# Optimization experiments

Hardware: AMD Instinct MI355X
Metric: run time of the kernel (lower is better)

## Reference

```python
import jax, jax.numpy as jnp
import numpy as np

B, S, DMODEL, HEADS = 2, 2048, 1024, 16
DK = DMODEL // HEADS
DV = DMODEL // HEADS


def setup_inputs() -> dict:
    key = jax.random.key(0)
    kx, kq, kk, kv = jax.random.split(key, 4)
    x = jax.random.normal(kx, (B, S, DMODEL), dtype=jnp.float32)
    # stacked per-head projection weights, shape [H, dmodel, dk/dv]
    # (equivalent to nn.Linear(dmodel, dk, bias=False) per head)
    scale = 1.0 / np.sqrt(DMODEL)
    Wq = jax.random.uniform(kq, (HEADS, DMODEL, DK), jnp.float32, -scale, scale)
    Wk = jax.random.uniform(kk, (HEADS, DMODEL, DK), jnp.float32, -scale, scale)
    Wv = jax.random.uniform(kv, (HEADS, DMODEL, DV), jnp.float32, -scale, scale)
    return {"x": x, "Wq": Wq, "Wk": Wk, "Wv": Wv}


def reference(x, Wq, Wk, Wv):
    # per-head projections, batched across heads: [B,H,S,dk]
    q = jnp.einsum("bsd,hdk->bhsk", x, Wq)
    k = jnp.einsum("bsd,hdk->bhsk", x, Wk)
    v = jnp.einsum("bsd,hdv->bhsv", x, Wv)
    # NOTE: original module applies NO 1/sqrt(dk) scaling — keep faithful
    scores = jnp.einsum("bhqk,bhsk->bhqs", q, k)  # [B,H,S,S]
    attn = jax.nn.softmax(scores, axis=-1)
    out = jnp.einsum("bhqs,bhsv->bhqv", attn, v)  # [B,H,S,dv]
    # concat heads along last dim in head order
    Bsz, H, Sq, Dv = out.shape
    return jnp.transpose(out, (0, 2, 1, 3)).reshape(Bsz, Sq, H * Dv)
```

## Files before the change

### kernel.cpp

```cpp
#include <hip/hip_runtime.h>

#define B_ 2
#define S_ 2048
#define D_ 1024
#define H_ 16
#define DK_ 64
#define M_ (B_ * S_)
#define N_ (3 * D_)

typedef __bf16 bf16x8 __attribute__((ext_vector_type(8)));
typedef short s8vec __attribute__((ext_vector_type(8)));
typedef float f4vec __attribute__((ext_vector_type(4)));

static __device__ __forceinline__ ushort f2b(float f) {
  union { float f; unsigned u; } v; v.f = f;
  unsigned u = v.u;
  u += 0x7FFFu + ((u >> 16) & 1u);
  return (ushort)(u >> 16);
}

static __device__ __forceinline__ unsigned pk2(float a, float b) {
#if __has_builtin(__builtin_amdgcn_cvt_pk_bf16_f32)
  typedef __bf16 b2 __attribute__((ext_vector_type(2)));
  b2 r = __builtin_amdgcn_cvt_pk_bf16_f32(a, b);
  return __builtin_bit_cast(unsigned, r);
#else
  return (unsigned)f2b(a) | ((unsigned)f2b(b) << 16);
#endif
}

static __device__ __forceinline__ float fexp2(float x) {
#if __has_builtin(__builtin_amdgcn_exp2f)
  return __builtin_amdgcn_exp2f(x);
#else
  return exp2f(x);
#endif
}

static __device__ __forceinline__ f4vec mfma16(s8vec a, s8vec b, f4vec c) {
  return __builtin_amdgcn_mfma_f32_16x16x32_bf16(
      __builtin_bit_cast(bf16x8, a), __builtin_bit_cast(bf16x8, b), c, 0, 0, 0);
}

static __device__ __forceinline__ void gl_lds16(const ushort* g, ushort* l) {
  __builtin_amdgcn_global_load_lds(
      (const __attribute__((address_space(1))) unsigned*)g,
      (__attribute__((address_space(3))) unsigned*)l, 16, 0, 0);
}

static __device__ __forceinline__ void wg_barrier_lds() {
  asm volatile("" ::: "memory");
  __builtin_amdgcn_s_waitcnt(0xC07F);
  __builtin_amdgcn_s_barrier();
  asm volatile("" ::: "memory");
}

__global__ __launch_bounds__(256) void cvt_all(const float* __restrict__ x,
                                               const float* __restrict__ Wq,
                                               const float* __restrict__ Wk,
                                               const float* __restrict__ Wv,
                                               ushort* __restrict__ xb,
                                               ushort* __restrict__ wbt) {
  const int t = threadIdx.x;
  if (blockIdx.x < 4096) {
    int i = blockIdx.x * 256 + t;
    float4 v = ((const float4*)x)[i];
    ushort4 o;
    o.x = f2b(v.x); o.y = f2b(v.y); o.z = f2b(v.z); o.w = f2b(v.w);
    ((ushort4*)xb)[i] = o;
  } else {
    __shared__ ushort T[64 * 72];
    int bid = blockIdx.x - 4096;
    int w = bid >> 8, rem = bid & 255;
    int h = rem >> 4, d0 = (rem & 15) * 64;
    const float* W = (w == 0) ? Wq : (w == 1) ? Wk : Wv;
    const float* src = W + (size_t)h * 65536 + (size_t)d0 * 64;
#pragma unroll
    for (int j = 0; j < 4; ++j) {
      int idx = j * 256 + t;
      int dr = idx >> 4, kc = (idx & 15) * 4;
      float4 v = *(const float4*)(src + dr * 64 + kc);
      T[(kc + 0) * 72 + dr] = f2b(v.x);
      T[(kc + 1) * 72 + dr] = f2b(v.y);
      T[(kc + 2) * 72 + dr] = f2b(v.z);
      T[(kc + 3) * 72 + dr] = f2b(v.w);
    }
    __syncthreads();
    const int kk = t >> 2, dcg = (t & 3) * 16;
    ushort* dst = wbt + ((size_t)w * 1024 + h * 64 + kk) * 1024 + d0 + dcg;
    *(s8vec*)dst       = *(const s8vec*)&T[kk * 72 + dcg];
    *(s8vec*)(dst + 8) = *(const s8vec*)&T[kk * 72 + dcg + 8];
  }
}

__global__ __launch_bounds__(256) void proj_gemm(const ushort* __restrict__ xb,
                                                 const ushort* __restrict__ wbt,
                                                 ushort* __restrict__ qkv) {
  __shared__ __attribute__((aligned(16))) ushort As[128 * 64];
  __shared__ __attribute__((aligned(16))) ushort Bs[128 * 64];
  const int tid = threadIdx.x, wid = tid >> 6, lane = tid & 63;
  const int quad = lane >> 4, l15 = lane & 15;
  const int wm = wid & 1, wn = wid >> 1;
  const int m0 = blockIdx.x * 128, n0 = blockIdx.y * 128;

  f4vec acc[4][4];
#pragma unroll
  for (int mb = 0; mb < 4; mb++)
#pragma unroll
    for (int nb = 0; nb < 4; nb++)
#pragma unroll
      for (int i = 0; i < 4; i++) acc[mb][nb][i] = 0.f;

  const int sr = tid >> 3, sg = tid & 7;
  const int lg = sg ^ (sr & 7);
  const ushort* Ab = xb + (size_t)m0 * D_;
  const ushort* Bb = wbt + (size_t)n0 * D_;

  for (int k0 = 0; k0 < D_; k0 += 64) {
    __syncthreads();
#pragma unroll
    for (int j = 0; j < 4; ++j) {
      int r = j * 32 + sr;
      gl_lds16(Ab + (size_t)r * D_ + k0 + lg * 8, &As[j * 2048 + wid * 512]);
      gl_lds16(Bb + (size_t)r * D_ + k0 + lg * 8, &Bs[j * 2048 + wid * 512]);
    }
    __syncthreads();

#pragma unroll
    for (int kb = 0; kb < 2; ++kb) {
      s8vec af[4], bf[4];
#pragma unroll
      for (int mb = 0; mb < 4; ++mb) {
        int m = wm * 64 + mb * 16 + l15;
        int gpos = (kb * 4 + quad) ^ (m & 7);
        af[mb] = *(const s8vec*)&As[m * 64 + gpos * 8];
      }
#pragma unroll
      for (int nb = 0; nb < 4; ++nb) {
        int n = wn * 64 + nb * 16 + l15;
        int gpos = (kb * 4 + quad) ^ (n & 7);
        bf[nb] = *(const s8vec*)&Bs[n * 64 + gpos * 8];
      }
#pragma unroll
      for (int mb = 0; mb < 4; ++mb)
#pragma unroll
        for (int nb = 0; nb < 4; ++nb)
          acc[mb][nb] = mfma16(af[mb], bf[nb], acc[mb][nb]);
    }
  }

  const size_t per = (size_t)B_ * H_ * S_ * DK_;
  const int w = n0 >> 10;
  if (w == 2) {
    ushort* vt = qkv + 2 * per;
#pragma unroll
    for (int mb = 0; mb < 4; ++mb)
#pragma unroll
      for (int nb = 0; nb < 4; ++nb)
#pragma unroll
        for (int i = 0; i < 4; ++i) {
          int m = m0 + wm * 64 + mb * 16 + quad * 4 + i;
          int b = m >> 11, s = m & 2047;
          int n1 = (n0 & 1023) + wn * 64 + nb * 16 + l15;
          vt[((size_t)b * 1024 + n1) * S_ + s] = f2b(acc[mb][nb][i]);
        }
  } else {
    const float qs = (w == 0) ? 1.44269504f : 1.0f;
#pragma unroll
    for (int mb = 0; mb < 4; ++mb)
#pragma unroll
      for (int nb = 0; nb < 4; ++nb)
#pragma unroll
        for (int i = 0; i < 4; ++i) {
          int m = m0 + wm * 64 + mb * 16 + quad * 4 + i;
          int b = m >> 11, s = m & 2047;
          int n1 = (n0 & 1023) + wn * 64 + nb * 16 + l15;
          qkv[(size_t)w * per + (((size_t)b * H_ + (n1 >> 6)) * S_ + s) * 64 + (n1 & 63)] =
              f2b(acc[mb][nb][i] * qs);
        }
  }
}

__global__ __launch_bounds__(256) void attn(const ushort* __restrict__ qg,
                                            const ushort* __restrict__ kg,
                                            const ushort* __restrict__ vtg,
                                            float* __restrict__ out) {
  __shared__ __attribute__((aligned(16))) ushort Ks[64 * 64];
  __shared__ __attribute__((aligned(16))) ushort Vt[64 * 64];
  __shared__ __attribute__((aligned(16))) ushort Ps[4][32 * 128];
  const int qt = blockIdx.x, bh = blockIdx.y;
  const int b = bh >> 4, h = bh & 15;
  const int tid = threadIdx.x, wid = tid >> 6, lane = tid & 63;
  const int quad = lane >> 4, l15 = lane & 15, l7 = l15 & 7;

  const ushort* qbase = qg + ((size_t)bh * S_ + qt * 128 + wid * 32) * DK_;
  s8vec aq[2][2];
#pragma unroll
  for (int mb = 0; mb < 2; mb++) {
    aq[mb][0] = *(const s8vec*)(qbase + (size_t)(mb * 16 + l15) * DK_ + quad * 8);
    aq[mb][1] = *(const s8vec*)(qbase + (size_t)(mb * 16 + l15) * DK_ + 32 + quad * 8);
  }

  f4vec o[2][4];
  float lsum[2];
#pragma unroll
  for (int mb = 0; mb < 2; mb++) {
    lsum[mb] = 0.f;
#pragma unroll
    for (int nb = 0; nb < 4; nb++)
#pragma unroll
      for (int i = 0; i < 4; i++) o[mb][nb][i] = 0.f;
  }

  const int r = tid >> 3, gs = tid & 7;
  const int gk = gs ^ (r & 7);
  const ushort* kb_ = kg + (size_t)bh * S_ * DK_;
  const ushort* vb_ = vtg + (size_t)bh * 64 * S_;

  s8vec kpre[2], vpre[2];
  kpre[0] = *(const s8vec*)(kb_ + (size_t)r * DK_ + gk * 8);
  kpre[1] = *(const s8vec*)(kb_ + (size_t)(r + 32) * DK_ + gk * 8);
  vpre[0] = *(const s8vec*)(vb_ + (size_t)r * S_ + gk * 8);
  vpre[1] = *(const s8vec*)(vb_ + (size_t)(r + 32) * S_ + gk * 8);

  for (int kt = 0; kt < S_ / 64; ++kt) {
    wg_barrier_lds();
    *(s8vec*)&Ks[r * 64 + gs * 8]        = kpre[0];
    *(s8vec*)&Ks[(r + 32) * 64 + gs * 8] = kpre[1];
    *(s8vec*)&Vt[r * 64 + gs * 8]        = vpre[0];
    *(s8vec*)&Vt[(r + 32) * 64 + gs * 8] = vpre[1];
    if (kt + 1 < S_ / 64) {
      const ushort* kn = kb_ + (size_t)((kt + 1) * 64 + r) * DK_ + gk * 8;
      kpre[0] = *(const s8vec*)(kn);
      kpre[1] = *(const s8vec*)(kn + (size_t)32 * DK_);
      const ushort* vn = vb_ + (size_t)r * S_ + (kt + 1) * 64 + gk * 8;
      vpre[0] = *(const s8vec*)(vn);
      vpre[1] = *(const s8vec*)(vn + (size_t)32 * S_);
    }
    wg_barrier_lds();

    f4vec sct[2][4];
#pragma unroll
    for (int nb = 0; nb < 4; nb++) {
      const int row = nb * 16 + l15;
      s8vec ak0 = *(const s8vec*)&Ks[row * 64 + ((0 + quad) ^ l7) * 8];
      s8vec ak1 = *(const s8vec*)&Ks[row * 64 + ((4 + quad) ^ l7) * 8];
#pragma unroll
      for (int mb = 0; mb < 2; mb++) {
        f4vec z;
#pragma unroll
        for (int i = 0; i < 4; i++) z[i] = 0.f;
        z = mfma16(ak0, aq[mb][0], z);
        sct[mb][nb] = mfma16(ak1, aq[mb][1], z);
      }
    }

#pragma unroll
    for (int mb = 0; mb < 2; mb++) {
      const int q = mb * 16 + l15;
#pragma unroll
      for (int nb = 0; nb < 4; nb++) {
#pragma unroll
        for (int i = 0; i < 4; i++) {
          float p = fexp2(sct[mb][nb][i]);
          sct[mb][nb][i] = p;
          lsum[mb] += p;
        }
        unsigned p01 = pk2(sct[mb][nb][0], sct[mb][nb][1]);
        unsigned p23 = pk2(sct[mb][nb][2], sct[mb][nb][3]);
        const int c = (nb * 2 + (quad >> 1)) ^ l7;
        *(uint2*)&Ps[wid][q * 128 + c * 8 + (quad & 1) * 4] = make_uint2(p01, p23);
      }
    }

#pragma unroll
    for (int kc = 0; kc < 2; kc++) {
      s8vec ap[2];
#pragma unroll
      for (int mb = 0; mb < 2; mb++)
        ap[mb] = *(const s8vec*)&Ps[wid][(mb * 16 + l15) * 128 + (((kc * 4 + quad)) ^ l7) * 8];
#pragma unroll
      for (int nb = 0; nb < 4; nb++) {
        s8vec av = *(const s8vec*)&Vt[(nb * 16 + l15) * 64 + ((kc * 4 + quad) ^ l7) * 8];
        o[0][nb] = mfma16(av, ap[0], o[0][nb]);
        o[1][nb] = mfma16(av, ap[1], o[1][nb]);
      }
    }
  }

#pragma unroll
  for (int mb = 0; mb < 2; mb++) {
    lsum[mb] += __shfl_xor(lsum[mb], 16, 64);
    lsum[mb] += __shfl_xor(lsum[mb], 32, 64);
  }

#pragma unroll
  for (int mb = 0; mb < 2; mb++) {
    const float inv = 1.0f / lsum[mb];
    float* ob = out + ((size_t)b * S_ + qt * 128 + wid * 32 + mb * 16 + l15) * D_ + h * DK_;
#pragma unroll
    for (int nb = 0; nb < 4; nb++) {
      float4 v;
      v.x = o[mb][nb][0] * inv;
      v.y = o[mb][nb][1] * inv;
      v.z = o[mb][nb][2] * inv;
      v.w = o[mb][nb][3] * inv;
      *(float4*)(ob + nb * 16 + quad * 4) = v;
    }
  }
}

extern "C" void kernel_launch(void* const* d_in, const int* in_sizes, int n_in,
                              void* d_out, int out_size, void* d_ws, size_t ws_size,
                              hipStream_t stream) {
  const float* x  = (const float*)d_in[0];
  const float* Wq = (const float*)d_in[1];
  const float* Wk = (const float*)d_in[2];
  const float* Wv = (const float*)d_in[3];
  float* out = (float*)d_out;

  ushort* xb  = (ushort*)d_ws;
  ushort* wbt = xb + (size_t)B_ * S_ * D_;
  ushort* qkv = wbt + (size_t)3 * D_ * D_;
  const size_t per = (size_t)B_ * H_ * S_ * DK_;

  cvt_all<<<4096 + 768, 256, 0, stream>>>(x, Wq, Wk, Wv, xb, wbt);
  proj_gemm<<<dim3(M_ / 128, N_ / 128), 256, 0, stream>>>(xb, wbt, qkv);
  attn<<<dim3(S_ / 128, B_ * H_), 256, 0, stream>>>(qkv, qkv + per, qkv + 2 * per, out);
}
```

Baseline: 177.5 us.

## Stage projection epilogue through LDS and shrink attention blocks with MFMA row sums

The projection GEMM epilogue now writes results into shared memory and then emits 16-byte coalesced stores for Q, K and the transposed V, replacing scattered 2-byte global stores. The attention kernel drops to 128 threads and 64 query rows per block, doubling the grid and cutting LDS use. It also computes the softmax denominator by appending a block of ones to V so an extra MFMA column yields the row sum, which removes the per-element scalar adds and the final shuffle reductions. The costs are one extra MFMA per V tile, smaller per-block reuse of each loaded K/V tile, and a changed workspace layout.

```diff
diff --git a/kernel.cpp b/kernel.cpp
--- a/kernel.cpp
+++ b/kernel.cpp
@@ -96,8 +96,9 @@
 __global__ __launch_bounds__(256) void proj_gemm(const ushort* __restrict__ xb,
                                                  const ushort* __restrict__ wbt,
                                                  ushort* __restrict__ qkv) {
-  __shared__ __attribute__((aligned(16))) ushort As[128 * 64];
-  __shared__ __attribute__((aligned(16))) ushort Bs[128 * 64];
+  __shared__ __attribute__((aligned(16))) ushort BUF[2 * 128 * 64];
+  ushort* As = BUF;
+  ushort* Bs = BUF + 128 * 64;
   const int tid = threadIdx.x, wid = tid >> 6, lane = tid & 63;
   const int quad = lane >> 4, l15 = lane & 15;
   const int wm = wid & 1, wn = wid >> 1;
@@ -149,51 +150,80 @@
     }
   }
 
+  __syncthreads();
+  ushort* T = BUF + wid * 4096;
   const size_t per = (size_t)B_ * H_ * S_ * DK_;
   const int w = n0 >> 10;
+  const int sb = m0 + wm * 64;
+  const int b = sb >> 11;
+  const int nb0 = (n0 & 1023) + wn * 64;
+
   if (w == 2) {
+#pragma unroll
+    for (int mb = 0; mb < 4; ++mb) {
+      const int mc = mb * 2 + (quad >> 1);
+      const int moff = (quad & 1) * 4;
+#pragma unroll
+      for (int nb = 0; nb < 4; ++nb) {
+        const int np = nb * 16 + l15;
+        unsigned p01 = pk2(acc[mb][nb][0], acc[mb][nb][1]);
+        unsigned p23 = pk2(acc[mb][nb][2], acc[mb][nb][3]);
+        *(uint2*)&T[np * 64 + ((mc ^ (np & 7)) * 8) + moff] = make_uint2(p01, p23);
+      }
+    }
     ushort* vt = qkv + 2 * per;
 #pragma unroll
-    for (int mb = 0; mb < 4; ++mb)
-#pragma unroll
-      for (int nb = 0; nb < 4; ++nb)
-#pragma unroll
-        for (int i = 0; i < 4; ++i) {
-          int m = m0 + wm * 64 + mb * 16 + quad * 4 + i;
-          int b = m >> 11, s = m & 2047;
-          int n1 = (n0 & 1023) + wn * 64 + nb * 16 + l15;
-          vt[((size_t)b * 1024 + n1) * S_ + s] = f2b(acc[mb][nb][i]);
-        }
+    for (int j = 0; j < 8; ++j) {
+      const int np = (lane >> 3) + j * 8;
+      const int mc2 = lane & 7;
+      s8vec v = *(const s8vec*)&T[np * 64 + ((mc2 ^ (np & 7)) * 8)];
+      const int n1 = nb0 + np;
+      *(s8vec*)(vt + ((size_t)b * 1024 + n1) * S_ + (sb & 2047) + mc2 * 8) = v;
+    }
   } else {
     const float qs = (w == 0) ? 1.44269504f : 1.0f;
 #pragma unroll
     for (int mb = 0; mb < 4; ++mb)
 #pragma unroll
-      for (int nb = 0; nb < 4; ++nb)
+      for (int nb = 0; nb < 4; ++nb) {
+        const int c = nb * 2 + (l15 >> 3);
 #pragma unroll
         for (int i = 0; i < 4; ++i) {
-          int m = m0 + wm * 64 + mb * 16 + quad * 4 + i;
-          int b = m >> 11, s = m & 2047;
-          int n1 = (n0 & 1023) + wn * 64 + nb * 16 + l15;
-          qkv[(size_t)w * per + (((size_t)b * H_ + (n1 >> 6)) * S_ + s) * 64 + (n1 & 63)] =
-              f2b(acc[mb][nb][i] * qs);
+          const int mp = mb * 16 + quad * 4 + i;
+          T[mp * 64 + ((c ^ (mp & 7)) * 8) + (l15 & 7)] = f2b(acc[mb][nb][i] * qs);
         }
-  }
-}
-
-__global__ __launch_bounds__(256) void attn(const ushort* __restrict__ qg,
+      }
+    const int h = nb0 >> 6;
+    ushort* qk = qkv + (size_t)w * per + (((size_t)b * H_ + h) * S_) * 64;
+#pragma unroll
+    for (int j = 0; j < 8; ++j) {
+      const int mp = (lane >> 3) + j * 8;
+      const int c2 = lane & 7;
+      s8vec v = *(const s8vec*)&T[mp * 64 + ((c2 ^ (mp & 7)) * 8)];
+      *(s8vec*)(qk + (size_t)((sb & 2047) + mp) * 64 + c2 * 8) = v;
+    }
+  }
+}
+
+__global__ __launch_bounds__(128) void attn(const ushort* __restrict__ qg,
                                             const ushort* __restrict__ kg,
                                             const ushort* __restrict__ vtg,
                                             float* __restrict__ out) {
   __shared__ __attribute__((aligned(16))) ushort Ks[64 * 64];
-  __shared__ __attribute__((aligned(16))) ushort Vt[64 * 64];
-  __shared__ __attribute__((aligned(16))) ushort Ps[4][32 * 128];
+  __shared__ __attribute__((aligned(16))) ushort Vt[80 * 64];
+  __shared__ __attribute__((aligned(16))) ushort Ps[2][32 * 64];
   const int qt = blockIdx.x, bh = blockIdx.y;
   const int b = bh >> 4, h = bh & 15;
   const int tid = threadIdx.x, wid = tid >> 6, lane = tid & 63;
   const int quad = lane >> 4, l15 = lane & 15, l7 = l15 & 7;
 
-  const ushort* qbase = qg + ((size_t)bh * S_ + qt * 128 + wid * 32) * DK_;
+  {
+    ushort* p = &Vt[(64 + (tid >> 3)) * 64 + (tid & 7) * 8];
+#pragma unroll
+    for (int j = 0; j < 8; ++j) p[j] = 0x3F80;
+  }
+
+  const ushort* qbase = qg + ((size_t)bh * S_ + qt * 64 + wid * 32) * DK_;
   s8vec aq[2][2];
 #pragma unroll
   for (int mb = 0; mb < 2; mb++) {
@@ -201,41 +231,41 @@
     aq[mb][1] = *(const s8vec*)(qbase + (size_t)(mb * 16 + l15) * DK_ + 32 + quad * 8);
   }
 
-  f4vec o[2][4];
-  float lsum[2];
-#pragma unroll
-  for (int mb = 0; mb < 2; mb++) {
-    lsum[mb] = 0.f;
-#pragma unroll
-    for (int nb = 0; nb < 4; nb++)
+  f4vec o[2][5];
+#pragma unroll
+  for (int mb = 0; mb < 2; mb++)
+#pragma unroll
+    for (int nb = 0; nb < 5; nb++)
 #pragma unroll
       for (int i = 0; i < 4; i++) o[mb][nb][i] = 0.f;
-  }
-
-  const int r = tid >> 3, gs = tid & 7;
-  const int gk = gs ^ (r & 7);
+
+  const int r0 = tid >> 3, gs = tid & 7;
+  const int gk = gs ^ (r0 & 7);
   const ushort* kb_ = kg + (size_t)bh * S_ * DK_;
   const ushort* vb_ = vtg + (size_t)bh * 64 * S_;
 
-  s8vec kpre[2], vpre[2];
-  kpre[0] = *(const s8vec*)(kb_ + (size_t)r * DK_ + gk * 8);
-  kpre[1] = *(const s8vec*)(kb_ + (size_t)(r + 32) * DK_ + gk * 8);
-  vpre[0] = *(const s8vec*)(vb_ + (size_t)r * S_ + gk * 8);
-  vpre[1] = *(const s8vec*)(vb_ + (size_t)(r + 32) * S_ + gk * 8);
+  s8vec kpre[4], vpre[4];
+#pragma unroll
+  for (int j = 0; j < 4; ++j) {
+    kpre[j] = *(const s8vec*)(kb_ + (size_t)(j * 16 + r0) * DK_ + gk * 8);
+    vpre[j] = *(const s8vec*)(vb_ + (size_t)(j * 16 + r0) * S_ + gk * 8);
+  }
 
   for (int kt = 0; kt < S_ / 64; ++kt) {
     wg_barrier_lds();
-    *(s8vec*)&Ks[r * 64 + gs * 8]        = kpre[0];
-    *(s8vec*)&Ks[(r + 32) * 64 + gs * 8] = kpre[1];
-    *(s8vec*)&Vt[r * 64 + gs * 8]        = vpre[0];
-    *(s8vec*)&Vt[(r + 32) * 64 + gs * 8] = vpre[1];
+#pragma unroll
+    for (int j = 0; j < 4; ++j) {
+      *(s8vec*)&Ks[(j * 16 + r0) * 64 + gs * 8] = kpre[j];
+      *(s8vec*)&Vt[(j * 16 + r0) * 64 + gs * 8] = vpre[j];
+    }
     if (kt + 1 < S_ / 64) {
-      const ushort* kn = kb_ + (size_t)((kt + 1) * 64 + r) * DK_ + gk * 8;
-      kpre[0] = *(const s8vec*)(kn);
-      kpre[1] = *(const s8vec*)(kn + (size_t)32 * DK_);
-      const ushort* vn = vb_ + (size_t)r * S_ + (kt + 1) * 64 + gk * 8;
-      vpre[0] = *(const s8vec*)(vn);
-      vpre[1] = *(const s8vec*)(vn + (size_t)32 * S_);
+      const ushort* kn = kb_ + (size_t)((kt + 1) * 64 + r0) * DK_ + gk * 8;
+      const ushort* vn = vb_ + (size_t)r0 * S_ + (kt + 1) * 64 + gk * 8;
+#pragma unroll
+      for (int j = 0; j < 4; ++j) {
+        kpre[j] = *(const s8vec*)(kn + (size_t)(j * 16) * DK_);
+        vpre[j] = *(const s8vec*)(vn + (size_t)(j * 16) * S_);
+      }
     }
     wg_barrier_lds();
 
@@ -260,16 +290,13 @@
       const int q = mb * 16 + l15;
 #pragma unroll
       for (int nb = 0; nb < 4; nb++) {
-#pragma unroll
-        for (int i = 0; i < 4; i++) {
-          float p = fexp2(sct[mb][nb][i]);
-          sct[mb][nb][i] = p;
-          lsum[mb] += p;
-        }
-        unsigned p01 = pk2(sct[mb][nb][0], sct[mb][nb][1]);
-        unsigned p23 = pk2(sct[mb][nb][2], sct[mb][nb][3]);
+        f4vec p;
+#pragma unroll
+        for (int i = 0; i < 4; i++) p[i] = fexp2(sct[mb][nb][i]);
+        unsigned p01 = pk2(p[0], p[1]);
+        unsigned p23 = pk2(p[2], p[3]);
         const int c = (nb * 2 + (quad >> 1)) ^ l7;
-        *(uint2*)&Ps[wid][q * 128 + c * 8 + (quad & 1) * 4] = make_uint2(p01, p23);
+        *(uint2*)&Ps[wid][q * 64 + c * 8 + (quad & 1) * 4] = make_uint2(p01, p23);
       }
     }
 
@@ -278,9 +305,9 @@
       s8vec ap[2];
 #pragma unroll
       for (int mb = 0; mb < 2; mb++)
-        ap[mb] = *(const s8vec*)&Ps[wid][(mb * 16 + l15) * 128 + (((kc * 4 + quad)) ^ l7) * 8];
-#pragma unroll
-      for (int nb = 0; nb < 4; nb++) {
+        ap[mb] = *(const s8vec*)&Ps[wid][(mb * 16 + l15) * 64 + ((kc * 4 + quad) ^ l7) * 8];
+#pragma unroll
+      for (int nb = 0; nb < 5; nb++) {
         s8vec av = *(const s8vec*)&Vt[(nb * 16 + l15) * 64 + ((kc * 4 + quad) ^ l7) * 8];
         o[0][nb] = mfma16(av, ap[0], o[0][nb]);
         o[1][nb] = mfma16(av, ap[1], o[1][nb]);
@@ -290,14 +317,8 @@
 
 #pragma unroll
   for (int mb = 0; mb < 2; mb++) {
-    lsum[mb] += __shfl_xor(lsum[mb], 16, 64);
-    lsum[mb] += __shfl_xor(lsum[mb], 32, 64);
-  }
-
-#pragma unroll
-  for (int mb = 0; mb < 2; mb++) {
-    const float inv = 1.0f / lsum[mb];
-    float* ob = out + ((size_t)b * S_ + qt * 128 + wid * 32 + mb * 16 + l15) * D_ + h * DK_;
+    const float inv = 1.0f / o[mb][4][0];
+    float* ob = out + ((size_t)b * S_ + qt * 64 + wid * 32 + mb * 16 + l15) * D_ + h * DK_;
 #pragma unroll
     for (int nb = 0; nb < 4; nb++) {
       float4 v;
@@ -319,12 +340,12 @@
   const float* Wv = (const float*)d_in[3];
   float* out = (float*)d_out;
 
-  ushort* xb  = (ushort*)d_ws;
+  ushort* qkv = (ushort*)d_ws;
+  const size_t per = (size_t)B_ * H_ * S_ * DK_;
+  ushort* xb  = qkv + 3 * per;
   ushort* wbt = xb + (size_t)B_ * S_ * D_;
-  ushort* qkv = wbt + (size_t)3 * D_ * D_;
-  const size_t per = (size_t)B_ * H_ * S_ * DK_;
 
   cvt_all<<<4096 + 768, 256, 0, stream>>>(x, Wq, Wk, Wv, xb, wbt);
   proj_gemm<<<dim3(M_ / 128, N_ / 128), 256, 0, stream>>>(xb, wbt, qkv);
-  attn<<<dim3(S_ / 128, B_ * H_), 256, 0, stream>>>(qkv, qkv + per, qkv + 2 * per, out);
-}
+  attn<<<dim3(S_ / 64, B_ * H_), 128, 0, stream>>>(qkv, qkv + per, qkv + 2 * per, out);
+}
```

Result: slower. 183.9 us (+3.6%).
